# Kernel optimization log

Hardware: AMD Instinct MI355X
Metric: run time of the kernel (lower is better)

Reference implementation:

```python
import jax, jax.numpy as jnp
import numpy as np
import math

D = 256
H = 8
HD = D // H
FF = 1024


def pos2posemb(pos, num_pos_feats=64, temperature=10000.0):
    scale = 2 * math.pi
    pos = pos * scale
    dim_t = jnp.arange(num_pos_feats, dtype=jnp.float32)
    dim_t = temperature ** (2.0 * jnp.floor(dim_t / 2) / num_pos_feats)
    pe = pos[..., None] / dim_t  # [N,4,64]
    pe = jnp.stack((jnp.sin(pe[..., 0::2]), jnp.cos(pe[..., 1::2])), axis=-1)  # [N,4,32,2]
    return pe.reshape(pe.shape[0], -1)  # [N,256]


def layer_norm(x, w, b, eps=1e-5):
    m = jnp.mean(x, axis=-1, keepdims=True)
    v = jnp.mean((x - m) ** 2, axis=-1, keepdims=True)
    return (x - m) * jax.lax.rsqrt(v + eps) * w + b


def setup_inputs() -> dict:
    key = jax.random.key(0)
    ks = jax.random.split(key, 24)
    N = 4096
    s = 0.02
    inp = {
        "ref_pts": jax.random.uniform(ks[0], (N, 4), jnp.float32),
        "pred_boxes": jax.random.uniform(ks[1], (N, 4), jnp.float32),
        "scores": jax.random.uniform(ks[2], (N,), jnp.float32),
        "output_embedding": jax.random.normal(ks[3], (N, D), jnp.float32),
        "query_pos": jax.random.normal(ks[4], (N, D), jnp.float32),
        "group_ids": jax.random.randint(ks[5], (N,), 0, 4, jnp.int64),
        "g_size": 4,
        "in_proj_w": jax.random.normal(ks[6], (3 * D, D), jnp.float32) * s,
        "in_proj_b": jnp.zeros((3 * D,), jnp.float32),
        "out_proj_w": jax.random.normal(ks[7], (D, D), jnp.float32) * s,
        "out_proj_b": jnp.zeros((D,), jnp.float32),
        "lin1_w": jax.random.normal(ks[8], (FF, D), jnp.float32) * s,
        "lin1_b": jnp.zeros((FF,), jnp.float32),
        "lin2_w": jax.random.normal(ks[9], (D, FF), jnp.float32) * s,
        "lin2_b": jnp.zeros((D,), jnp.float32),
        "feat1_w": jax.random.normal(ks[10], (FF, D), jnp.float32) * s,
        "feat1_b": jnp.zeros((FF,), jnp.float32),
        "feat2_w": jax.random.normal(ks[11], (D, FF), jnp.float32) * s,
        "feat2_b": jnp.zeros((D,), jnp.float32),
        "norm1_w": jnp.ones((D,), jnp.float32),
        "norm1_b": jnp.zeros((D,), jnp.float32),
        "norm2_w": jnp.ones((D,), jnp.float32),
        "norm2_b": jnp.zeros((D,), jnp.float32),
        "normf_w": jnp.ones((D,), jnp.float32),
        "normf_b": jnp.zeros((D,), jnp.float32),
    }
    return inp


def reference(ref_pts, pred_boxes, scores, output_embedding, query_pos,
              in_proj_w, in_proj_b, out_proj_w, out_proj_b,
              lin1_w, lin1_b, lin2_w, lin2_b,
              feat1_w, feat1_b, feat2_w, feat2_b,
              norm1_w, norm1_b, norm2_w, norm2_b, normf_w, normf_b,
              group_ids, g_size):
    N = ref_pts.shape[0]
    is_pos = scores > 0.5  # score_thr = 0.5
    # ref_pts[is_pos] = pred_boxes.detach()[is_pos]
    ref = jnp.where(is_pos[:, None], jax.lax.stop_gradient(pred_boxes), ref_pts)

    out_embed = output_embedding
    qpos_emb = pos2posemb(ref)  # [N,256]
    qk = qpos_emb + out_embed

    # grouped block-diagonal mask: 0 within same group, -inf across groups
    mask = jnp.where(group_ids[:, None] == group_ids[None, :], 0.0, -jnp.inf)

    # MultiheadAttention (eval, dropout=0)
    q = qk @ in_proj_w[:D].T + in_proj_b[:D]
    k = qk @ in_proj_w[D:2 * D].T + in_proj_b[D:2 * D]
    v = out_embed @ in_proj_w[2 * D:].T + in_proj_b[2 * D:]
    qh = q.reshape(N, H, HD)
    kh = k.reshape(N, H, HD)
    vh = v.reshape(N, H, HD)
    logits = jnp.einsum("nhd,mhd->hnm", qh, kh) / jnp.sqrt(jnp.float32(HD)) + mask
    attn = jax.nn.softmax(logits, axis=-1)
    ctx = jnp.einsum("hnm,mhd->nhd", attn, vh).reshape(N, D)
    tgt2 = ctx @ out_proj_w.T + out_proj_b

    tgt = layer_norm(out_embed + tgt2, norm1_w, norm1_b)
    ffn = jax.nn.relu(tgt @ lin1_w.T + lin1_b) @ lin2_w.T + lin2_b
    tgt = layer_norm(tgt + ffn, norm2_w, norm2_b)

    feat = jax.nn.relu(tgt @ feat1_w.T + feat1_b) @ feat2_w.T + feat2_b
    query_feat = layer_norm(query_pos + feat, normf_w, normf_b)

    # query_pos[is_pos] = query_feat[is_pos]
    query_pos_out = jnp.where(is_pos[:, None], query_feat, query_pos)
    return query_pos_out
```

## Files before the change

### kernel.cpp

```cpp
#include <hip/hip_runtime.h>


typedef __attribute__((ext_vector_type(8))) __bf16 bf16x8;
typedef __attribute__((ext_vector_type(4))) float f32x4;

#define NSPLIT 2

static __device__ __forceinline__ unsigned short f2bf(float f) {
    union { float f; unsigned u; } v; v.f = f;
    unsigned r = v.u + 0x7fffu + ((v.u >> 16) & 1u);
    return (unsigned short)(r >> 16);
}

__global__ __launch_bounds__(1024) void k_setup(
    const float* __restrict__ w0, const float* __restrict__ w1,
    const float* __restrict__ w2, const float* __restrict__ w3,
    const float* __restrict__ w4, const float* __restrict__ w5,
    unsigned short* __restrict__ o0, unsigned short* __restrict__ o1,
    unsigned short* __restrict__ o2, unsigned short* __restrict__ o3,
    unsigned short* __restrict__ o4, unsigned short* __restrict__ o5,
    const int* __restrict__ gid, int N,
    int* __restrict__ perm, int* __restrict__ rank,
    int* __restrict__ gid_s, int* __restrict__ offs)
{
    if (blockIdx.x < 320) {
        long i = ((long)blockIdx.x * 1024 + threadIdx.x) * 4;
        const float* src; unsigned short* dst; long off;
        if      (i <  196608) { src = w0; dst = o0; off = i; }
        else if (i <  262144) { src = w1; dst = o1; off = i -  196608; }
        else if (i <  524288) { src = w2; dst = o2; off = i -  262144; }
        else if (i <  786432) { src = w3; dst = o3; off = i -  524288; }
        else if (i < 1048576) { src = w4; dst = o4; off = i -  786432; }
        else                  { src = w5; dst = o5; off = i - 1048576; }
        float4 v = *(const float4*)(src + off);
        ushort4 o; o.x = f2bf(v.x); o.y = f2bf(v.y); o.z = f2bf(v.z); o.w = f2bf(v.w);
        *(ushort4*)(dst + off) = o;
        return;
    }
    __shared__ int cnt[1024][4];
    __shared__ int base[4];
    int t = threadIdx.x;
    int per = N / 1024;
    int c[4] = {0, 0, 0, 0};
    for (int i = 0; i < per; ++i) c[gid[t * per + i] & 3]++;
    for (int g = 0; g < 4; ++g) cnt[t][g] = c[g];
    __syncthreads();
    for (int off = 1; off < 1024; off <<= 1) {
        int v[4] = {0, 0, 0, 0};
        if (t >= off) for (int g = 0; g < 4; ++g) v[g] = cnt[t - off][g];
        __syncthreads();
        if (t >= off) for (int g = 0; g < 4; ++g) cnt[t][g] += v[g];
        __syncthreads();
    }
    if (t == 0) {
        base[0] = 0;
        base[1] = cnt[1023][0];
        base[2] = base[1] + cnt[1023][1];
        base[3] = base[2] + cnt[1023][2];
        offs[0] = 0; offs[1] = base[1]; offs[2] = base[2]; offs[3] = base[3]; offs[4] = N;
    }
    __syncthreads();
    int run[4];
    for (int g = 0; g < 4; ++g) run[g] = base[g] + (t ? cnt[t - 1][g] : 0);
    for (int i = 0; i < per; ++i) {
        int n = t * per + i;
        int g = gid[n] & 3;
        int p = run[g]++;
        perm[p] = n; rank[n] = p; gid_s[p] = g;
    }
}

__global__ __launch_bounds__(256) void k_prep(
    const float* __restrict__ ref_pts, const float* __restrict__ pred_boxes,
    const float* __restrict__ scores, const float* __restrict__ embed,
    const float* __restrict__ qpos, const int* __restrict__ rank,
    unsigned short* __restrict__ qk_bf, unsigned short* __restrict__ emb_bf,
    float* __restrict__ emb_f32s, float* __restrict__ qpos_s,
    float* __restrict__ scores_s)
{
    int n = blockIdx.x, d = threadIdx.x;
    int pos = rank[n];
    bool ip = scores[n] > 0.5f;
    int c = d >> 6, k = (d >> 1) & 31, s = d & 1;
    float p = (ip ? pred_boxes : ref_pts)[n * 4 + c] * 6.283185307179586f;
    float freq = exp2f(-(float)k * (13.287712379549449f / 32.0f));
    float ang = p * freq;
    float e = s ? cosf(ang) : sinf(ang);
    float em = embed[(size_t)n * 256 + d];
    qk_bf[(size_t)pos * 256 + d] = f2bf(e + em);
    emb_bf[(size_t)pos * 256 + d] = f2bf(em);
    emb_f32s[(size_t)pos * 256 + d] = em;
    qpos_s[(size_t)pos * 256 + d] = qpos[(size_t)n * 256 + d];
    if (d == 0) scores_s[pos] = scores[n];
}

#define EPI_QKV     0
#define EPI_RELUBF  3

template<int EPI>
__global__ __launch_bounds__(256) void k_gemm(
    const unsigned short* __restrict__ A, const unsigned short* __restrict__ A2,
    const unsigned short* __restrict__ B,
    const float* __restrict__ bias,
    void* __restrict__ out, void* __restrict__ out2,
    int M, int Nout, int K)
{
    __shared__ __align__(16) unsigned short As[2][64][72];
    __shared__ __align__(16) unsigned short Bs[2][64][72];
    int mt = M >> 6;
    int bm = blockIdx.x % mt, bn = blockIdx.x / mt;
    int m0 = bm * 64, c0 = bn * 64;
    int tid = threadIdx.x;
    int wave = tid >> 6, lane = tid & 63;
    int wr = wave >> 1, wc = wave & 1;
    int g = lane >> 4, r15 = lane & 15;

    const unsigned short* Asrc = A;
    if constexpr (EPI == EPI_QKV) { if (c0 >= 512) Asrc = A2; }

    int r0 = tid >> 3, u0 = tid & 7;
    int r1 = 32 + (tid >> 3), u1 = tid & 7;

    const unsigned short* Abase = Asrc + (size_t)m0 * K;
    const unsigned short* Bbase = B + (size_t)c0 * K;

    uint4 a0 = *(const uint4*)(Abase + (size_t)r0 * K + u0 * 8);
    uint4 a1 = *(const uint4*)(Abase + (size_t)r1 * K + u1 * 8);
    uint4 b0 = *(const uint4*)(Bbase + (size_t)r0 * K + u0 * 8);
    uint4 b1 = *(const uint4*)(Bbase + (size_t)r1 * K + u1 * 8);
    *(uint4*)(&As[0][r0][u0 * 8]) = a0;
    *(uint4*)(&As[0][r1][u1 * 8]) = a1;
    *(uint4*)(&Bs[0][r0][u0 * 8]) = b0;
    *(uint4*)(&Bs[0][r1][u1 * 8]) = b1;
    __syncthreads();

    f32x4 acc[2][2] = {};
    int nk = K >> 6;
    for (int kt = 0; kt < nk; ++kt) {
        int cur = kt & 1;
        bool more = (kt + 1 < nk);
        if (more) {
            int kc = (kt + 1) << 6;
            a0 = *(const uint4*)(Abase + (size_t)r0 * K + kc + u0 * 8);
            a1 = *(const uint4*)(Abase + (size_t)r1 * K + kc + u1 * 8);
            b0 = *(const uint4*)(Bbase + (size_t)r0 * K + kc + u0 * 8);
            b1 = *(const uint4*)(Bbase + (size_t)r1 * K + kc + u1 * 8);
        }
        #pragma unroll
        for (int kk = 0; kk < 2; ++kk) {
            bf16x8 af0 = *(const bf16x8*)(&As[cur][wr * 32 + r15][kk * 32 + g * 8]);
            bf16x8 af1 = *(const bf16x8*)(&As[cur][wr * 32 + 16 + r15][kk * 32 + g * 8]);
            bf16x8 bf0 = *(const bf16x8*)(&Bs[cur][wc * 32 + r15][kk * 32 + g * 8]);
            bf16x8 bf1 = *(const bf16x8*)(&Bs[cur][wc * 32 + 16 + r15][kk * 32 + g * 8]);
            acc[0][0] = __builtin_amdgcn_mfma_f32_16x16x32_bf16(af0, bf0, acc[0][0], 0, 0, 0);
            acc[0][1] = __builtin_amdgcn_mfma_f32_16x16x32_bf16(af0, bf1, acc[0][1], 0, 0, 0);
            acc[1][0] = __builtin_amdgcn_mfma_f32_16x16x32_bf16(af1, bf0, acc[1][0], 0, 0, 0);
            acc[1][1] = __builtin_amdgcn_mfma_f32_16x16x32_bf16(af1, bf1, acc[1][1], 0, 0, 0);
        }
        if (more) {
            *(uint4*)(&As[cur ^ 1][r0][u0 * 8]) = a0;
            *(uint4*)(&As[cur ^ 1][r1][u1 * 8]) = a1;
            *(uint4*)(&Bs[cur ^ 1][r0][u0 * 8]) = b0;
            *(uint4*)(&Bs[cur ^ 1][r1][u1 * 8]) = b1;
            __syncthreads();
        }
    }

    #pragma unroll
    for (int ti = 0; ti < 2; ++ti)
    #pragma unroll
    for (int tj = 0; tj < 2; ++tj)
    #pragma unroll
    for (int r = 0; r < 4; ++r) {
        int n = m0 + wr * 32 + ti * 16 + g * 4 + r;
        int o = c0 + wc * 32 + tj * 16 + r15;
        float v = acc[ti][tj][r] + bias[o];
        if constexpr (EPI == EPI_QKV) {
            if (o < 512) {
                float s = (o < 256) ? (0.17677669529663687f * 1.4426950408889634f) : 1.0f;
                ((unsigned short*)out)[(size_t)n * 512 + o] = f2bf(v * s);
            } else {
                ((unsigned short*)out2)[(size_t)(o - 512) * M + n] = f2bf(v);
            }
        } else {
            ((unsigned short*)out)[(size_t)n * Nout + o] = f2bf(fmaxf(v, 0.0f));
        }
    }
}

template<int K, int MODE>
__global__ __launch_bounds__(256) void k_gemmln(
    const unsigned short* __restrict__ Abf,
    const float* __restrict__ Opart, const float* __restrict__ lpart,
    const unsigned short* __restrict__ Bw,
    const float* __restrict__ bias, const float* __restrict__ resid,
    const float* __restrict__ lnw, const float* __restrict__ lnb,
    float* __restrict__ outf32, unsigned short* __restrict__ outbf,
    const float* __restrict__ scores_s, const int* __restrict__ perm, int N)
{
    __shared__ __align__(16) unsigned short As[2][64][72];
    __shared__ __align__(16) unsigned short Bs[2][256][72];
    __shared__ float sW[64][65];
    __shared__ float qW[64][65];
    __shared__ float mS[64], rS[64];

    const int m0 = blockIdx.x * 64;
    const int tid = threadIdx.x, wave = tid >> 6, lane = tid & 63;
    const int g = lane >> 4, r15 = lane & 15;

    const int ar0 = tid >> 3, ar1 = 32 + (tid >> 3), au = tid & 7;
    int bR[8];
    #pragma unroll
    for (int i = 0; i < 8; ++i) bR[i] = i * 32 + (tid >> 3);

    auto loadA = [&](int kt, int r) -> uint4 {
        int n = m0 + r;
        int c = kt * 64 + au * 8;
        if constexpr (MODE == 0) {
            int h = c >> 5;
            float l0 = lpart[(size_t)n * 8 + h];
            float l1 = lpart[((size_t)N + n) * 8 + h];
            float inv = 1.0f / (l0 + l1);
            const float* p0 = Opart + (size_t)n * 256 + c;
            const float* p1 = Opart + ((size_t)N + n) * 256 + c;
            float4 x0 = *(const float4*)(p0);
            float4 x1 = *(const float4*)(p0 + 4);
            float4 y0 = *(const float4*)(p1);
            float4 y1 = *(const float4*)(p1 + 4);
            unsigned e0 = f2bf((x0.x + y0.x) * inv) | ((unsigned)f2bf((x0.y + y0.y) * inv) << 16);
            unsigned e1 = f2bf((x0.z + y0.z) * inv) | ((unsigned)f2bf((x0.w + y0.w) * inv) << 16);
            unsigned e2 = f2bf((x1.x + y1.x) * inv) | ((unsigned)f2bf((x1.y + y1.y) * inv) << 16);
            unsigned e3 = f2bf((x1.z + y1.z) * inv) | ((unsigned)f2bf((x1.w + y1.w) * inv) << 16);
            uint4 o; o.x = e0; o.y = e1; o.z = e2; o.w = e3;
            return o;
        } else {
            return *(const uint4*)(Abf + (size_t)n * K + c);
        }
    };

    uint4 pa0 = loadA(0, ar0);
    uint4 pa1 = loadA(0, ar1);
    uint4 pb[8];
    #pragma unroll
    for (int i = 0; i < 8; ++i)
        pb[i] = *(const uint4*)(Bw + (size_t)bR[i] * K + au * 8);
    *(uint4*)(&As[0][ar0][au * 8]) = pa0;
    *(uint4*)(&As[0][ar1][au * 8]) = pa1;
    #pragma unroll
    for (int i = 0; i < 8; ++i)
        *(uint4*)(&Bs[0][bR[i]][au * 8]) = pb[i];
    __syncthreads();

    f32x4 acc[4][4] = {};
    constexpr int nk = K >> 6;
    for (int kt = 0; kt < nk; ++kt) {
        int cur = kt & 1;
        bool more = (kt + 1 < nk);
        if (more) {
            int kc = (kt + 1) << 6;
            pa0 = loadA(kt + 1, ar0);
            pa1 = loadA(kt + 1, ar1);
            #pragma unroll
            for (int i = 0; i < 8; ++i)
                pb[i] = *(const uint4*)(Bw + (size_t)bR[i] * K + kc + au * 8);
        }
        #pragma unroll
        for (int kk = 0; kk < 2; ++kk) {
            bf16x8 af[4], bfr[4];
            #pragma unroll
            for (int ti = 0; ti < 4; ++ti)
                af[ti] = *(const bf16x8*)(&As[cur][ti * 16 + r15][kk * 32 + g * 8]);
            #pragma unroll
            for (int tj = 0; tj < 4; ++tj)
                bfr[tj] = *(const bf16x8*)(&Bs[cur][wave * 64 + tj * 16 + r15][kk * 32 + g * 8]);
            #pragma unroll
            for (int ti = 0; ti < 4; ++ti)
                #pragma unroll
                for (int tj = 0; tj < 4; ++tj)
                    acc[ti][tj] = __builtin_amdgcn_mfma_f32_16x16x32_bf16(af[ti], bfr[tj], acc[ti][tj], 0, 0, 0);
        }
        if (more) {
            *(uint4*)(&As[cur ^ 1][ar0][au * 8]) = pa0;
            *(uint4*)(&As[cur ^ 1][ar1][au * 8]) = pa1;
            #pragma unroll
            for (int i = 0; i < 8; ++i)
                *(uint4*)(&Bs[cur ^ 1][bR[i]][au * 8]) = pb[i];
            __syncthreads();
        }
    }

    float sp_[4][4] = {}, qp_[4][4] = {};
    #pragma unroll
    for (int ti = 0; ti < 4; ++ti)
    #pragma unroll
    for (int tj = 0; tj < 4; ++tj)
    #pragma unroll
    for (int r = 0; r < 4; ++r) {
        int n = ti * 16 + g * 4 + r;
        int col = wave * 64 + tj * 16 + r15;
        float v = acc[ti][tj][r] + bias[col] + resid[(size_t)(m0 + n) * 256 + col];
        acc[ti][tj][r] = v;
        sp_[ti][r] += v;
        qp_[ti][r] += v * v;
    }
    #pragma unroll
    for (int ti = 0; ti < 4; ++ti)
    #pragma unroll
    for (int r = 0; r < 4; ++r) {
        int n = ti * 16 + g * 4 + r;
        sW[n][wave * 16 + r15] = sp_[ti][r];
        qW[n][wave * 16 + r15] = qp_[ti][r];
    }
    __syncthreads();
    {
        int n = tid >> 2, seg = tid & 3;
        float s = 0.f, q = 0.f;
        #pragma unroll
        for (int j = 0; j < 16; ++j) { s += sW[n][seg * 16 + j]; q += qW[n][seg * 16 + j]; }
        s += __shfl_xor(s, 1, 64); s += __shfl_xor(s, 2, 64);
        q += __shfl_xor(q, 1, 64); q += __shfl_xor(q, 2, 64);
        if (seg == 0) {
            float mean = s * (1.0f / 256.0f);
            float var = q * (1.0f / 256.0f) - mean * mean;
            mS[n] = mean;
            rS[n] = rsqrtf(fmaxf(var, 0.f) + 1e-5f);
        }
    }
    __syncthreads();

    #pragma unroll
    for (int ti = 0; ti < 4; ++ti)
    #pragma unroll
    for (int tj = 0; tj < 4; ++tj)
    #pragma unroll
    for (int r = 0; r < 4; ++r) {
        int n = ti * 16 + g * 4 + r;
        int col = wave * 64 + tj * 16 + r15;
        float o = (acc[ti][tj][r] - mS[n]) * rS[n] * lnw[col] + lnb[col];
        if constexpr (MODE == 0) {
            outf32[(size_t)(m0 + n) * 256 + col] = o;
            outbf[(size_t)(m0 + n) * 256 + col] = f2bf(o);
        } else if constexpr (MODE == 1) {
            outbf[(size_t)(m0 + n) * 256 + col] = f2bf(o);
        } else {
            bool ip = scores_s[m0 + n] > 0.5f;
            float qp = resid[(size_t)(m0 + n) * 256 + col];
            int no = perm[m0 + n];
            outf32[(size_t)no * 256 + col] = ip ? o : qp;
        }
    }
}

__global__ __launch_bounds__(256) void k_attn(
    const unsigned short* __restrict__ QK, const unsigned short* __restrict__ Vt,
    const int* __restrict__ gid_s, const int* __restrict__ offs,
    float* __restrict__ Opart, float* __restrict__ lpart, int N)
{
    __shared__ __align__(16) unsigned short Ks[2][64][40];
    __shared__ __align__(16) unsigned short Vs[2][32][72];
    __shared__ __align__(16) unsigned short Ps[4][16][64];
    __shared__ __align__(16) int gks[2][64];

    int qtiles = N >> 6;
    int bid = blockIdx.x;
    int qt = bid % qtiles;
    int hs = bid / qtiles;
    int h = hs & 7;
    int sp = hs >> 3;
    int q0 = qt * 64;
    int tid = threadIdx.x, wave = tid >> 6, lane = tid & 63;
    int g = lane >> 4, r15 = lane & 15;
    int n0 = q0 + wave * 16;

    int g_lo = gid_s[q0], g_hi = gid_s[q0 + 63];
    int tlo = offs[g_lo] >> 6;
    int thi = (offs[g_hi + 1] + 63) >> 6;
    int ntiles = thi - tlo;
    int chunk = (ntiles + NSPLIT - 1) / NSPLIT;
    int t0 = tlo + sp * chunk;
    int t1 = min(t0 + chunk, thi);

    if (t0 >= t1) {
        #pragma unroll
        for (int r = 0; r < 4; ++r) {
            int n = n0 + g * 4 + r;
            Opart[((size_t)sp * N + n) * 256 + h * 32 + r15] = 0.f;
            Opart[((size_t)sp * N + n) * 256 + h * 32 + 16 + r15] = 0.f;
        }
        if (g == 0) lpart[((size_t)sp * N + n0 + r15) * 8 + h] = 0.f;
        return;
    }

    bf16x8 qf = *(const bf16x8*)(QK + (size_t)(n0 + r15) * 512 + h * 32 + g * 8);
    int gq = gid_s[n0 + r15];

    int kr_ = tid >> 2, kc_ = (tid & 3) * 8;
    int vd_ = tid >> 3, vc_ = (tid & 7) * 8;

    f32x4 O0 = {}, O1 = {};
    float lloc = 0.f;
    unsigned short* PsW = &Ps[wave][0][0];

    {
        int m0 = t0 << 6;
        *(uint4*)(&Ks[0][kr_][kc_]) = *(const uint4*)(QK + (size_t)(m0 + kr_) * 512 + 256 + h * 32 + kc_);
        *(uint4*)(&Vs[0][vd_][vc_]) = *(const uint4*)(Vt + (size_t)(h * 32 + vd_) * N + m0 + vc_);
        if (tid < 64) gks[0][tid] = gid_s[m0 + tid];
    }
    __syncthreads();

    int cur = 0;
    for (int t = t0; t < t1; ++t) {
        bool more = (t + 1 < t1);
        uint4 kn, vn; int gn = 0;
        if (more) {
            int m0n = (t + 1) << 6;
            kn = *(const uint4*)(QK + (size_t)(m0n + kr_) * 512 + 256 + h * 32 + kc_);
            vn = *(const uint4*)(Vt + (size_t)(h * 32 + vd_) * N + m0n + vc_);
            if (tid < 64) gn = gid_s[m0n + tid];
        }

        f32x4 S[4];
        #pragma unroll
        for (int t_ = 0; t_ < 4; ++t_) {
            bf16x8 kf = *(const bf16x8*)(&Ks[cur][t_ * 16 + r15][g * 8]);
            f32x4 z = {};
            S[t_] = __builtin_amdgcn_mfma_f32_16x16x32_bf16(kf, qf, z, 0, 0, 0);
        }
        #pragma unroll
        for (int t_ = 0; t_ < 4; ++t_) {
            int4 g4 = *(const int4*)(&gks[cur][t_ * 16 + g * 4]);
            float p0 = (g4.x == gq) ? exp2f(S[t_][0]) : 0.f;
            float p1 = (g4.y == gq) ? exp2f(S[t_][1]) : 0.f;
            float p2 = (g4.z == gq) ? exp2f(S[t_][2]) : 0.f;
            float p3 = (g4.w == gq) ? exp2f(S[t_][3]) : 0.f;
            lloc += (p0 + p1) + (p2 + p3);
            ushort4 pw;
            pw.x = f2bf(p0); pw.y = f2bf(p1); pw.z = f2bf(p2); pw.w = f2bf(p3);
            int off = t_ * 32 + g * 8;
            int byte = r15 * 128 + ((((off >> 4) ^ (r15 & 7)) << 4) | (off & 15));
            *(ushort4*)((char*)PsW + byte) = pw;
        }
        #pragma unroll
        for (int kk = 0; kk < 2; ++kk) {
            int byte = r15 * 128 + (((kk * 4 + g) ^ (r15 & 7)) << 4);
            bf16x8 pf = *(const bf16x8*)((char*)PsW + byte);
            bf16x8 v0 = *(const bf16x8*)(&Vs[cur][r15][kk * 32 + g * 8]);
            bf16x8 v1 = *(const bf16x8*)(&Vs[cur][16 + r15][kk * 32 + g * 8]);
            O0 = __builtin_amdgcn_mfma_f32_16x16x32_bf16(pf, v0, O0, 0, 0, 0);
            O1 = __builtin_amdgcn_mfma_f32_16x16x32_bf16(pf, v1, O1, 0, 0, 0);
        }

        if (more) {
            *(uint4*)(&Ks[cur ^ 1][kr_][kc_]) = kn;
            *(uint4*)(&Vs[cur ^ 1][vd_][vc_]) = vn;
            if (tid < 64) gks[cur ^ 1][tid] = gn;
        }
        __syncthreads();
        cur ^= 1;
    }

    float l = lloc;
    l += __shfl_xor(l, 16, 64);
    l += __shfl_xor(l, 32, 64);
    if (g == 0) lpart[((size_t)sp * N + n0 + r15) * 8 + h] = l;

    #pragma unroll
    for (int r = 0; r < 4; ++r) {
        int n = n0 + g * 4 + r;
        Opart[((size_t)sp * N + n) * 256 + h * 32 + r15]      = O0[r];
        Opart[((size_t)sp * N + n) * 256 + h * 32 + 16 + r15] = O1[r];
    }
}

extern "C" void kernel_launch(void* const* d_in, const int* in_sizes, int n_in,
                              void* d_out, int out_size, void* d_ws, size_t ws_size,
                              hipStream_t stream)
{
    const float* ref_pts    = (const float*)d_in[0];
    const float* pred_boxes = (const float*)d_in[1];
    const float* scores     = (const float*)d_in[2];
    const float* out_embed  = (const float*)d_in[3];
    const float* query_pos  = (const float*)d_in[4];
    const int*   group_ids  = (const int*)d_in[5];
    const float* in_proj_w  = (const float*)d_in[7];
    const float* in_proj_b  = (const float*)d_in[8];
    const float* out_proj_w = (const float*)d_in[9];
    const float* out_proj_b = (const float*)d_in[10];
    const float* lin1_w     = (const float*)d_in[11];
    const float* lin1_b     = (const float*)d_in[12];
    const float* lin2_w     = (const float*)d_in[13];
    const float* lin2_b     = (const float*)d_in[14];
    const float* feat1_w    = (const float*)d_in[15];
    const float* feat1_b    = (const float*)d_in[16];
    const float* feat2_w    = (const float*)d_in[17];
    const float* feat2_b    = (const float*)d_in[18];
    const float* norm1_w    = (const float*)d_in[19];
    const float* norm1_b    = (const float*)d_in[20];
    const float* norm2_w    = (const float*)d_in[21];
    const float* norm2_b    = (const float*)d_in[22];
    const float* normf_w    = (const float*)d_in[23];
    const float* normf_b    = (const float*)d_in[24];

    const int N = in_sizes[2];

    char* ws = (char*)d_ws;
    size_t off = 0;
    auto alloc = [&](size_t bytes) -> void* {
        void* p = ws + off; off += (bytes + 255) & ~(size_t)255; return p;
    };
    unsigned short* wqkv   = (unsigned short*)alloc((size_t)768 * 256 * 2);
    unsigned short* wout   = (unsigned short*)alloc((size_t)256 * 256 * 2);
    unsigned short* wlin1  = (unsigned short*)alloc((size_t)1024 * 256 * 2);
    unsigned short* wlin2  = (unsigned short*)alloc((size_t)256 * 1024 * 2);
    unsigned short* wfeat1 = (unsigned short*)alloc((size_t)1024 * 256 * 2);
    unsigned short* wfeat2 = (unsigned short*)alloc((size_t)256 * 1024 * 2);
    unsigned short* qk_bf  = (unsigned short*)alloc((size_t)N * 256 * 2);
    unsigned short* emb_bf = (unsigned short*)alloc((size_t)N * 256 * 2);
    unsigned short* QKbuf  = (unsigned short*)alloc((size_t)N * 512 * 2);
    unsigned short* Vtbuf  = (unsigned short*)alloc((size_t)256 * N * 2);
    float*          tgtf   = (float*)alloc((size_t)N * 256 * 4);
    unsigned short* tgtbf  = (unsigned short*)alloc((size_t)N * 256 * 2);
    unsigned short* t2bf   = (unsigned short*)alloc((size_t)N * 256 * 2);
    unsigned short* hbuf   = (unsigned short*)alloc((size_t)N * 1024 * 2);
    float* emb_f32s = (float*)alloc((size_t)N * 256 * 4);
    float* qpos_s   = (float*)alloc((size_t)N * 256 * 4);
    float* scores_s = (float*)alloc((size_t)N * 4);
    int* permbuf = (int*)alloc((size_t)N * 4);
    int* rankbuf = (int*)alloc((size_t)N * 4);
    int* gidsbuf = (int*)alloc((size_t)N * 4);
    int* offsbuf = (int*)alloc(32 * 4);
    float* Opartbuf = (float*)alloc((size_t)NSPLIT * N * 256 * 4);
    float* lbuf     = (float*)alloc((size_t)NSPLIT * N * 8 * 4);
    (void)ws_size; (void)n_in; (void)out_size;

    const int mt = N >> 6;

    k_setup<<<321, 1024, 0, stream>>>(in_proj_w, out_proj_w, lin1_w, lin2_w, feat1_w, feat2_w,
                                      wqkv, wout, wlin1, wlin2, wfeat1, wfeat2,
                                      group_ids, N, permbuf, rankbuf, gidsbuf, offsbuf);
    k_prep<<<N, 256, 0, stream>>>(ref_pts, pred_boxes, scores, out_embed, query_pos, rankbuf,
                                  qk_bf, emb_bf, emb_f32s, qpos_s, scores_s);
    k_gemm<EPI_QKV><<<mt * 12, 256, 0, stream>>>(
        qk_bf, emb_bf, wqkv, in_proj_b, QKbuf, Vtbuf, N, 768, 256);
    k_attn<<<mt * 8 * NSPLIT, 256, 0, stream>>>(QKbuf, Vtbuf, gidsbuf, offsbuf,
                                                Opartbuf, lbuf, N);
    k_gemmln<256, 0><<<mt, 256, 0, stream>>>(
        nullptr, Opartbuf, lbuf, wout, out_proj_b, emb_f32s,
        norm1_w, norm1_b, tgtf, tgtbf, nullptr, nullptr, N);
    k_gemm<EPI_RELUBF><<<mt * 16, 256, 0, stream>>>(
        tgtbf, nullptr, wlin1, lin1_b, hbuf, nullptr, N, 1024, 256);
    k_gemmln<1024, 1><<<mt, 256, 0, stream>>>(
        hbuf, nullptr, nullptr, wlin2, lin2_b, tgtf,
        norm2_w, norm2_b, nullptr, t2bf, nullptr, nullptr, N);
    k_gemm<EPI_RELUBF><<<mt * 16, 256, 0, stream>>>(
        t2bf, nullptr, wfeat1, feat1_b, hbuf, nullptr, N, 1024, 256);
    k_gemmln<1024, 2><<<mt, 256, 0, stream>>>(
        hbuf, nullptr, nullptr, wfeat2, feat2_b, qpos_s,
        normf_w, normf_b, (float*)d_out, nullptr, scores_s, permbuf, N);
}
```

Measured before the change: 135.0 us.

## Shrink GEMM+LayerNorm row tile to 16 and stream B directly into registers

The fused GEMM+LayerNorm kernel now processes 16 rows per block instead of 64, so it launches 256 blocks instead of 64 on a GPU with many more compute units. B fragments are loaded from global memory straight into registers and double-buffered there, with no shared-memory staging. Row statistics are reduced with wave shuffles, which replaces the larger shared-memory reduction. In exchange, B reuse across rows drops fourfold, so each block rereads the whole weight matrix and L2 traffic rises.

```diff
diff --git a/kernel.cpp b/kernel.cpp
--- a/kernel.cpp
+++ b/kernel.cpp
@@ -198,23 +198,20 @@
     float* __restrict__ outf32, unsigned short* __restrict__ outbf,
     const float* __restrict__ scores_s, const int* __restrict__ perm, int N)
 {
-    __shared__ __align__(16) unsigned short As[2][64][72];
-    __shared__ __align__(16) unsigned short Bs[2][256][72];
-    __shared__ float sW[64][65];
-    __shared__ float qW[64][65];
-    __shared__ float mS[64], rS[64];
-
-    const int m0 = blockIdx.x * 64;
+    __shared__ __align__(16) unsigned short As[2][16][72];
+    __shared__ float sW[4][16];
+    __shared__ float qW[4][16];
+    __shared__ float mS[16], rS[16];
+
+    const int m0 = blockIdx.x * 16;
     const int tid = threadIdx.x, wave = tid >> 6, lane = tid & 63;
     const int g = lane >> 4, r15 = lane & 15;
 
-    const int ar0 = tid >> 3, ar1 = 32 + (tid >> 3), au = tid & 7;
-    int bR[8];
-    #pragma unroll
-    for (int i = 0; i < 8; ++i) bR[i] = i * 32 + (tid >> 3);
-
-    auto loadA = [&](int kt, int r) -> uint4 {
-        int n = m0 + r;
+    const int ar = tid >> 3, au = tid & 7;
+    const bool stager = (tid < 128);
+
+    auto loadA = [&](int kt) -> uint4 {
+        int n = m0 + ar;
         int c = kt * 64 + au * 8;
         if constexpr (MODE == 0) {
             int h = c >> 5;
@@ -227,126 +224,114 @@
             float4 x1 = *(const float4*)(p0 + 4);
             float4 y0 = *(const float4*)(p1);
             float4 y1 = *(const float4*)(p1 + 4);
-            unsigned e0 = f2bf((x0.x + y0.x) * inv) | ((unsigned)f2bf((x0.y + y0.y) * inv) << 16);
-            unsigned e1 = f2bf((x0.z + y0.z) * inv) | ((unsigned)f2bf((x0.w + y0.w) * inv) << 16);
-            unsigned e2 = f2bf((x1.x + y1.x) * inv) | ((unsigned)f2bf((x1.y + y1.y) * inv) << 16);
-            unsigned e3 = f2bf((x1.z + y1.z) * inv) | ((unsigned)f2bf((x1.w + y1.w) * inv) << 16);
-            uint4 o; o.x = e0; o.y = e1; o.z = e2; o.w = e3;
+            uint4 o;
+            o.x = f2bf((x0.x + y0.x) * inv) | ((unsigned)f2bf((x0.y + y0.y) * inv) << 16);
+            o.y = f2bf((x0.z + y0.z) * inv) | ((unsigned)f2bf((x0.w + y0.w) * inv) << 16);
+            o.z = f2bf((x1.x + y1.x) * inv) | ((unsigned)f2bf((x1.y + y1.y) * inv) << 16);
+            o.w = f2bf((x1.z + y1.z) * inv) | ((unsigned)f2bf((x1.w + y1.w) * inv) << 16);
             return o;
         } else {
             return *(const uint4*)(Abf + (size_t)n * K + c);
         }
     };
 
-    uint4 pa0 = loadA(0, ar0);
-    uint4 pa1 = loadA(0, ar1);
-    uint4 pb[8];
-    #pragma unroll
-    for (int i = 0; i < 8; ++i)
-        pb[i] = *(const uint4*)(Bw + (size_t)bR[i] * K + au * 8);
-    *(uint4*)(&As[0][ar0][au * 8]) = pa0;
-    *(uint4*)(&As[0][ar1][au * 8]) = pa1;
-    #pragma unroll
-    for (int i = 0; i < 8; ++i)
-        *(uint4*)(&Bs[0][bR[i]][au * 8]) = pb[i];
-    __syncthreads();
-
-    f32x4 acc[4][4] = {};
+    const unsigned short* Bb = Bw + (size_t)(wave * 64 + r15) * K + g * 8;
+#define LOADB(dst, kt, kk, tj) dst = *(const bf16x8*)(Bb + (size_t)(tj) * 16 * K + (kt) * 64 + (kk) * 32)
+
+    bf16x8 c00, c01, c02, c03, c10, c11, c12, c13;
+    uint4 pa;
+    if (stager) { pa = loadA(0); *(uint4*)(&As[0][ar][au * 8]) = pa; }
+    LOADB(c00, 0, 0, 0); LOADB(c01, 0, 0, 1); LOADB(c02, 0, 0, 2); LOADB(c03, 0, 0, 3);
+    LOADB(c10, 0, 1, 0); LOADB(c11, 0, 1, 1); LOADB(c12, 0, 1, 2); LOADB(c13, 0, 1, 3);
+    __syncthreads();
+
+    f32x4 acc[4] = {};
     constexpr int nk = K >> 6;
     for (int kt = 0; kt < nk; ++kt) {
         int cur = kt & 1;
         bool more = (kt + 1 < nk);
+        bf16x8 n00, n01, n02, n03, n10, n11, n12, n13;
         if (more) {
-            int kc = (kt + 1) << 6;
-            pa0 = loadA(kt + 1, ar0);
-            pa1 = loadA(kt + 1, ar1);
-            #pragma unroll
-            for (int i = 0; i < 8; ++i)
-                pb[i] = *(const uint4*)(Bw + (size_t)bR[i] * K + kc + au * 8);
-        }
-        #pragma unroll
-        for (int kk = 0; kk < 2; ++kk) {
-            bf16x8 af[4], bfr[4];
-            #pragma unroll
-            for (int ti = 0; ti < 4; ++ti)
-                af[ti] = *(const bf16x8*)(&As[cur][ti * 16 + r15][kk * 32 + g * 8]);
-            #pragma unroll
-            for (int tj = 0; tj < 4; ++tj)
-                bfr[tj] = *(const bf16x8*)(&Bs[cur][wave * 64 + tj * 16 + r15][kk * 32 + g * 8]);
-            #pragma unroll
-            for (int ti = 0; ti < 4; ++ti)
-                #pragma unroll
-                for (int tj = 0; tj < 4; ++tj)
-                    acc[ti][tj] = __builtin_amdgcn_mfma_f32_16x16x32_bf16(af[ti], bfr[tj], acc[ti][tj], 0, 0, 0);
-        }
+            if (stager) pa = loadA(kt + 1);
+            LOADB(n00, kt + 1, 0, 0); LOADB(n01, kt + 1, 0, 1);
+            LOADB(n02, kt + 1, 0, 2); LOADB(n03, kt + 1, 0, 3);
+            LOADB(n10, kt + 1, 1, 0); LOADB(n11, kt + 1, 1, 1);
+            LOADB(n12, kt + 1, 1, 2); LOADB(n13, kt + 1, 1, 3);
+        }
+        bf16x8 af0 = *(const bf16x8*)(&As[cur][r15][g * 8]);
+        acc[0] = __builtin_amdgcn_mfma_f32_16x16x32_bf16(af0, c00, acc[0], 0, 0, 0);
+        acc[1] = __builtin_amdgcn_mfma_f32_16x16x32_bf16(af0, c01, acc[1], 0, 0, 0);
+        acc[2] = __builtin_amdgcn_mfma_f32_16x16x32_bf16(af0, c02, acc[2], 0, 0, 0);
+        acc[3] = __builtin_amdgcn_mfma_f32_16x16x32_bf16(af0, c03, acc[3], 0, 0, 0);
+        bf16x8 af1 = *(const bf16x8*)(&As[cur][r15][32 + g * 8]);
+        acc[0] = __builtin_amdgcn_mfma_f32_16x16x32_bf16(af1, c10, acc[0], 0, 0, 0);
+        acc[1] = __builtin_amdgcn_mfma_f32_16x16x32_bf16(af1, c11, acc[1], 0, 0, 0);
+        acc[2] = __builtin_amdgcn_mfma_f32_16x16x32_bf16(af1, c12, acc[2], 0, 0, 0);
+        acc[3] = __builtin_amdgcn_mfma_f32_16x16x32_bf16(af1, c13, acc[3], 0, 0, 0);
         if (more) {
-            *(uint4*)(&As[cur ^ 1][ar0][au * 8]) = pa0;
-            *(uint4*)(&As[cur ^ 1][ar1][au * 8]) = pa1;
-            #pragma unroll
-            for (int i = 0; i < 8; ++i)
-                *(uint4*)(&Bs[cur ^ 1][bR[i]][au * 8]) = pb[i];
+            if (stager) *(uint4*)(&As[cur ^ 1][ar][au * 8]) = pa;
             __syncthreads();
-        }
-    }
-
-    float sp_[4][4] = {}, qp_[4][4] = {};
-    #pragma unroll
-    for (int ti = 0; ti < 4; ++ti)
-    #pragma unroll
-    for (int tj = 0; tj < 4; ++tj)
-    #pragma unroll
-    for (int r = 0; r < 4; ++r) {
-        int n = ti * 16 + g * 4 + r;
+            c00 = n00; c01 = n01; c02 = n02; c03 = n03;
+            c10 = n10; c11 = n11; c12 = n12; c13 = n13;
+        }
+    }
+#undef LOADB
+
+    float vals[4][4];
+    float vs[4] = {0.f, 0.f, 0.f, 0.f}, vq[4] = {0.f, 0.f, 0.f, 0.f};
+    #pragma unroll
+    for (int tj = 0; tj < 4; ++tj) {
         int col = wave * 64 + tj * 16 + r15;
-        float v = acc[ti][tj][r] + bias[col] + resid[(size_t)(m0 + n) * 256 + col];
-        acc[ti][tj][r] = v;
-        sp_[ti][r] += v;
-        qp_[ti][r] += v * v;
-    }
-    #pragma unroll
-    for (int ti = 0; ti < 4; ++ti)
-    #pragma unroll
-    for (int r = 0; r < 4; ++r) {
-        int n = ti * 16 + g * 4 + r;
-        sW[n][wave * 16 + r15] = sp_[ti][r];
-        qW[n][wave * 16 + r15] = qp_[ti][r];
-    }
-    __syncthreads();
-    {
-        int n = tid >> 2, seg = tid & 3;
-        float s = 0.f, q = 0.f;
-        #pragma unroll
-        for (int j = 0; j < 16; ++j) { s += sW[n][seg * 16 + j]; q += qW[n][seg * 16 + j]; }
-        s += __shfl_xor(s, 1, 64); s += __shfl_xor(s, 2, 64);
-        q += __shfl_xor(q, 1, 64); q += __shfl_xor(q, 2, 64);
-        if (seg == 0) {
-            float mean = s * (1.0f / 256.0f);
-            float var = q * (1.0f / 256.0f) - mean * mean;
-            mS[n] = mean;
-            rS[n] = rsqrtf(fmaxf(var, 0.f) + 1e-5f);
-        }
-    }
-    __syncthreads();
-
-    #pragma unroll
-    for (int ti = 0; ti < 4; ++ti)
-    #pragma unroll
-    for (int tj = 0; tj < 4; ++tj)
-    #pragma unroll
-    for (int r = 0; r < 4; ++r) {
-        int n = ti * 16 + g * 4 + r;
+        float b = bias[col];
+        #pragma unroll
+        for (int r = 0; r < 4; ++r) {
+            int row = g * 4 + r;
+            float v = acc[tj][r] + b + resid[(size_t)(m0 + row) * 256 + col];
+            vals[tj][r] = v;
+            vs[r] += v; vq[r] += v * v;
+        }
+    }
+    #pragma unroll
+    for (int off = 1; off < 16; off <<= 1)
+        #pragma unroll
+        for (int r = 0; r < 4; ++r) {
+            vs[r] += __shfl_xor(vs[r], off, 64);
+            vq[r] += __shfl_xor(vq[r], off, 64);
+        }
+    if (r15 == 0) {
+        #pragma unroll
+        for (int r = 0; r < 4; ++r) { sW[wave][g * 4 + r] = vs[r]; qW[wave][g * 4 + r] = vq[r]; }
+    }
+    __syncthreads();
+    if (tid < 16) {
+        float s = sW[0][tid] + sW[1][tid] + sW[2][tid] + sW[3][tid];
+        float q = qW[0][tid] + qW[1][tid] + qW[2][tid] + qW[3][tid];
+        float mean = s * (1.0f / 256.0f);
+        float var = q * (1.0f / 256.0f) - mean * mean;
+        mS[tid] = mean;
+        rS[tid] = rsqrtf(fmaxf(var, 0.f) + 1e-5f);
+    }
+    __syncthreads();
+
+    #pragma unroll
+    for (int tj = 0; tj < 4; ++tj) {
         int col = wave * 64 + tj * 16 + r15;
-        float o = (acc[ti][tj][r] - mS[n]) * rS[n] * lnw[col] + lnb[col];
-        if constexpr (MODE == 0) {
-            outf32[(size_t)(m0 + n) * 256 + col] = o;
-            outbf[(size_t)(m0 + n) * 256 + col] = f2bf(o);
-        } else if constexpr (MODE == 1) {
-            outbf[(size_t)(m0 + n) * 256 + col] = f2bf(o);
-        } else {
-            bool ip = scores_s[m0 + n] > 0.5f;
-            float qp = resid[(size_t)(m0 + n) * 256 + col];
-            int no = perm[m0 + n];
-            outf32[(size_t)no * 256 + col] = ip ? o : qp;
+        float w = lnw[col], bb = lnb[col];
+        #pragma unroll
+        for (int r = 0; r < 4; ++r) {
+            int row = g * 4 + r;
+            float o = (vals[tj][r] - mS[row]) * rS[row] * w + bb;
+            if constexpr (MODE == 0) {
+                outf32[(size_t)(m0 + row) * 256 + col] = o;
+                outbf[(size_t)(m0 + row) * 256 + col] = f2bf(o);
+            } else if constexpr (MODE == 1) {
+                outbf[(size_t)(m0 + row) * 256 + col] = f2bf(o);
+            } else {
+                bool ip = scores_s[m0 + row] > 0.5f;
+                float qp = resid[(size_t)(m0 + row) * 256 + col];
+                int no = perm[m0 + row];
+                outf32[(size_t)no * 256 + col] = ip ? o : qp;
+            }
         }
     }
 }
@@ -545,17 +530,17 @@
         qk_bf, emb_bf, wqkv, in_proj_b, QKbuf, Vtbuf, N, 768, 256);
     k_attn<<<mt * 8 * NSPLIT, 256, 0, stream>>>(QKbuf, Vtbuf, gidsbuf, offsbuf,
                                                 Opartbuf, lbuf, N);
-    k_gemmln<256, 0><<<mt, 256, 0, stream>>>(
+    k_gemmln<256, 0><<<N / 16, 256, 0, stream>>>(
         nullptr, Opartbuf, lbuf, wout, out_proj_b, emb_f32s,
         norm1_w, norm1_b, tgtf, tgtbf, nullptr, nullptr, N);
     k_gemm<EPI_RELUBF><<<mt * 16, 256, 0, stream>>>(
         tgtbf, nullptr, wlin1, lin1_b, hbuf, nullptr, N, 1024, 256);
-    k_gemmln<1024, 1><<<mt, 256, 0, stream>>>(
+    k_gemmln<1024, 1><<<N / 16, 256, 0, stream>>>(
         hbuf, nullptr, nullptr, wlin2, lin2_b, tgtf,
         norm2_w, norm2_b, nullptr, t2bf, nullptr, nullptr, N);
     k_gemm<EPI_RELUBF><<<mt * 16, 256, 0, stream>>>(
         t2bf, nullptr, wfeat1, feat1_b, hbuf, nullptr, N, 1024, 256);
-    k_gemmln<1024, 2><<<mt, 256, 0, stream>>>(
+    k_gemmln<1024, 2><<<N / 16, 256, 0, stream>>>(
         hbuf, nullptr, nullptr, wfeat2, feat2_b, qpos_s,
         normf_w, normf_b, (float*)d_out, nullptr, scores_s, permbuf, N);
 }
```

After: 123.4 us. 1.09x faster.
